# Optimization experiments

Measured on AMD Instinct MI355X. Metric: run time of the kernel, lower is better.

## Reference

```python
import jax, jax.numpy as jnp
import numpy as np

EMA_DECAY = 0.99
LAPLACE_EPS = 1e-7
PERPLEXITY_EPS = 1e-10
COMMIT_COEF = 0.25


def setup_inputs() -> dict:
    key = jax.random.key(0)
    k1, k2, k3, k4 = jax.random.split(key, 4)
    B, C, T, H, W = 8, 256, 4, 32, 32
    n_codes = 2048
    z = jax.random.normal(k1, (B, C, T, H, W), dtype=jnp.float32)
    embeddings = jax.random.normal(k2, (n_codes, C), dtype=jnp.float32)
    N = jnp.ones((n_codes,), dtype=jnp.float32)  # state after _init_embeddings
    z_avg = jax.random.normal(k3, (n_codes, C), dtype=jnp.float32)
    k_rand = jax.random.normal(k4, (n_codes, C), dtype=jnp.float32)  # stand-in for randperm restart rows
    return {"z": z, "embeddings": embeddings, "N": N, "z_avg": z_avg, "k_rand": k_rand}


def reference(z, embeddings, N, z_avg, k_rand):
    b, c, t, h, w = z.shape
    n_codes = embeddings.shape[0]
    # rearrange 'b c t h w -> (b t h w) c'
    flat = jnp.transpose(z, (0, 2, 3, 4, 1)).reshape(-1, c)  # [Ntok, c]
    d2 = ((flat * flat).sum(axis=1, keepdims=True)
          - 2.0 * (flat @ embeddings.T)
          + (embeddings * embeddings).sum(axis=1)[None, :])  # [Ntok, n_codes]
    idx = jnp.argmin(d2, axis=1)  # [Ntok] int
    quant_flat = embeddings[idx]  # gather, [Ntok, c]
    # back to [b, c, t, h, w] (the double-rearrange in the torch code is a net permute back)
    quant = jnp.transpose(quant_flat.reshape(b, t, h, w, c), (0, 4, 1, 2, 3))
    commitment_loss = COMMIT_COEF * jnp.mean((z - jax.lax.stop_gradient(quant)) ** 2)
    embeddings_st = jax.lax.stop_gradient(quant - z) + z  # straight-through
    # EMA codebook update (one-hot scatter expressed as segment_sum)
    ones = jnp.ones(flat.shape[0], dtype=flat.dtype)
    counts = jax.ops.segment_sum(ones, idx, num_segments=n_codes)          # n_total
    encode_sum = jax.ops.segment_sum(flat, idx, num_segments=n_codes)      # [n_codes, c]
    new_N = N * EMA_DECAY + (1.0 - EMA_DECAY) * counts
    new_z_avg = z_avg * EMA_DECAY + (1.0 - EMA_DECAY) * encode_sum
    n = new_N.sum()
    weights = (new_N + LAPLACE_EPS) / (n + n_codes * LAPLACE_EPS) * n
    new_embeddings = new_z_avg / weights[:, None]
    usage = (new_N[:, None] >= 1.0).astype(flat.dtype)
    new_embeddings = new_embeddings * usage + k_rand * (1.0 - usage)
    # perplexity
    avg_probs = counts / flat.shape[0]
    perplexity = jnp.exp(-jnp.sum(avg_probs * jnp.log(avg_probs + PERPLEXITY_EPS)))
    encodings = idx.reshape(b, t, h, w)
    return embeddings_st, encodings, commitment_loss, perplexity, new_embeddings, new_N, new_z_avg
```

## Files before the change

kernel.cpp:

```cpp
#include <hip/hip_runtime.h>
#include <math.h>

#define NCODES 2048
#define CDIM   256
#define SPAT   4096
#define NTOK   32768
#define XSTR   260
#define EPI_TOK 32

#define ETILE    32
#define HALFCODE 1024
#define NTILES   (HALFCODE / ETILE)

typedef _Float16 half8  __attribute__((ext_vector_type(8)));
typedef float    f32x4  __attribute__((ext_vector_type(4)));

#define WS_ENORM  0
#define WS_COUNTS 2048
#define WS_LOSS   4096
#define WS_N      4097
#define WS_ESUM   4100
#define WS_IDX    528388
#define WS_OFF    561156
#define WS_CUR    563204
#define WS_SORT   565252
#define WS_SCODE  598020
#define WS_CAND   630788
#define WS_E16    761860
#define WS_XH     1024004

#define O_QUANT 0
#define O_ENC   8388608
#define O_LOSS  8421376
#define O_PERP  8421377
#define O_EMB   8421378
#define O_NN    8945666
#define O_ZAVG  8947714

__device__ inline void gl_lds16(const void* g, void* l) {
    __builtin_amdgcn_global_load_lds(
        (const __attribute__((address_space(1))) void*)g,
        (__attribute__((address_space(3))) void*)l, 16, 0, 0);
}

__device__ inline unsigned umn(unsigned a, unsigned b) { return a < b ? a : b; }
__device__ inline unsigned umx(unsigned a, unsigned b) { return a > b ? a : b; }
__device__ inline unsigned shflx16(unsigned v, int off) {
    return (unsigned)__shfl_xor((int)v, off, 16);
}

__global__ void k_ecvt(const float* __restrict__ emb, float* __restrict__ ws) {
    const int tid  = threadIdx.x;
    const int code = (blockIdx.x << 3) + (tid >> 5);
    const int cg   = tid & 31;
    const float* src = emb + (size_t)code * CDIM + (cg << 3);
    const float4 f0 = *(const float4*)src;
    const float4 f1 = *(const float4*)(src + 4);
    half8 h = { (_Float16)f0.x, (_Float16)f0.y, (_Float16)f0.z, (_Float16)f0.w,
                (_Float16)f1.x, (_Float16)f1.y, (_Float16)f1.z, (_Float16)f1.w };
    char* dst = (char*)(ws + WS_E16) + (size_t)code * 512 + ((cg ^ (code & 7)) << 4);
    *(half8*)dst = h;
    float s = f0.x * f0.x + f0.y * f0.y + f0.z * f0.z + f0.w * f0.w
            + f1.x * f1.x + f1.y * f1.y + f1.z * f1.z + f1.w * f1.w;
#pragma unroll
    for (int off = 16; off; off >>= 1) s += __shfl_down(s, off, 32);
    if (cg == 0) ws[WS_ENORM + code] = s;
}

__global__ __launch_bounds__(256, 3) void k_main(
    const float* __restrict__ z, float* __restrict__ ws)
{
    __shared__ half8 Es8[2][ETILE][32];

    const int tid = threadIdx.x;
    const int blk = blockIdx.x;
    const int ch  = blk & 1;
    const int tb  = blk >> 1;
    const int b   = tb >> 5;
    const int s0  = (tb & 31) * 128;
    const float* zb = z + (size_t)b * CDIM * SPAT + s0;
    const char* e16g = (const char*)(ws + WS_E16) + (size_t)ch * HALFCODE * 512;

    const int l  = tid & 63, w = tid >> 6;
    const int lr = l & 15, lg = l >> 4;

    {
        char* dst = (char*)&Es8[0][0][0];
#pragma unroll
        for (int q = 0; q < 4; ++q) {
            const int off = ((q << 2) + w) << 10;
            gl_lds16(e16g + off + (l << 4), dst + off);
        }
    }

    half8 a[2][8];
#pragma unroll
    for (int as = 0; as < 2; ++as)
#pragma unroll
    for (int ks = 0; ks < 8; ++ks) {
        float v[8];
#pragma unroll
        for (int e = 0; e < 8; ++e)
            v[e] = zb[(size_t)(ks * 32 + lg * 8 + e) * SPAT + (w * 32 + as * 16 + lr)];
        half8 h = { (_Float16)v[0], (_Float16)v[1], (_Float16)v[2], (_Float16)v[3],
                    (_Float16)v[4], (_Float16)v[5], (_Float16)v[6], (_Float16)v[7] };
        a[as][ks] = h;
    }

    unsigned kb0[2][4], kb1[2][4];
#pragma unroll
    for (int as = 0; as < 2; ++as)
#pragma unroll
    for (int r = 0; r < 4; ++r) { kb0[as][r] = 0xFFFFFFFFu; kb1[as][r] = 0xFFFFFFFFu; }

    __syncthreads();

    int p = 0;
    for (int tile = 0; tile < NTILES; ++tile) {
        if (tile < NTILES - 1) {
            const char* src = e16g + (size_t)(tile + 1) * (ETILE * 512);
            char* dst = (char*)&Es8[p ^ 1][0][0];
#pragma unroll
            for (int q = 0; q < 4; ++q) {
                const int off = ((q << 2) + w) << 10;
                gl_lds16(src + off + (l << 4), dst + off);
            }
        }

        const float en0 = ws[WS_ENORM + ch * HALFCODE + tile * ETILE + lr];
        const float en1 = ws[WS_ENORM + ch * HALFCODE + tile * ETILE + 16 + lr];

        f32x4 acc[2][2];
#pragma unroll
        for (int as = 0; as < 2; ++as)
#pragma unroll
        for (int j = 0; j < 2; ++j) acc[as][j] = (f32x4)0.0f;

        half8 bf0[2], bf1[2];
#pragma unroll
        for (int j = 0; j < 2; ++j) {
            const int row = j * 16 + lr;
            bf0[j] = Es8[p][row][lg ^ (row & 7)];
        }
#pragma unroll
        for (int ks = 0; ks < 8; ++ks) {
            if (ks < 7) {
#pragma unroll
                for (int j = 0; j < 2; ++j) {
                    const int row = j * 16 + lr;
                    if (ks & 1) bf0[j] = Es8[p][row][((ks + 1) * 4 + lg) ^ (row & 7)];
                    else        bf1[j] = Es8[p][row][((ks + 1) * 4 + lg) ^ (row & 7)];
                }
            }
            __builtin_amdgcn_s_setprio(1);
#pragma unroll
            for (int as = 0; as < 2; ++as)
#pragma unroll
            for (int j = 0; j < 2; ++j)
                acc[as][j] = __builtin_amdgcn_mfma_f32_16x16x32_f16(
                    a[as][ks], (ks & 1) ? bf1[j] : bf0[j], acc[as][j], 0, 0, 0);
            __builtin_amdgcn_s_setprio(0);
        }

        const float enb0 = en0 + 4096.0f;
        const float enb1 = en1 + 4096.0f;
        const unsigned code0 = (unsigned)(ch * HALFCODE + tile * ETILE + lr);
        const unsigned code1 = code0 + 16u;
#pragma unroll
        for (int as = 0; as < 2; ++as)
#pragma unroll
        for (int r = 0; r < 4; ++r) {
            {
                const float d = fmaf(acc[as][0][r], -2.0f, enb0);
                const unsigned key = (__float_as_uint(d) & 0xFFFFF800u) | code0;
                const unsigned hi = umx(kb0[as][r], key);
                kb0[as][r] = umn(kb0[as][r], key);
                kb1[as][r] = umn(kb1[as][r], hi);
            }
            {
                const float d = fmaf(acc[as][1][r], -2.0f, enb1);
                const unsigned key = (__float_as_uint(d) & 0xFFFFF800u) | code1;
                const unsigned hi = umx(kb0[as][r], key);
                kb0[as][r] = umn(kb0[as][r], key);
                kb1[as][r] = umn(kb1[as][r], hi);
            }
        }

        __syncthreads();
        p ^= 1;
    }

#pragma unroll
    for (int as = 0; as < 2; ++as)
#pragma unroll
    for (int r = 0; r < 4; ++r) {
        unsigned k0 = kb0[as][r], k1 = kb1[as][r];
        unsigned k2 = 0xFFFFFFFFu, k3 = 0xFFFFFFFFu;
#pragma unroll
        for (int off = 8; off; off >>= 1) {
            const unsigned o0 = shflx16(k0, off);
            const unsigned o1 = shflx16(k1, off);
            const unsigned o2 = shflx16(k2, off);
            const unsigned o3 = shflx16(k3, off);
            const unsigned m0 = umn(k0, o3), m1 = umn(k1, o2);
            const unsigned m2 = umn(k2, o1), m3 = umn(k3, o0);
            const unsigned t0 = umn(m0, m2), t2 = umx(m0, m2);
            const unsigned t1 = umn(m1, m3), t3 = umx(m1, m3);
            k0 = umn(t0, t1); k1 = umx(t0, t1);
            k2 = umn(t2, t3); k3 = umx(t2, t3);
        }
        if (lr == 0) {
            const int tokg = b * SPAT + s0 + w * 32 + as * 16 + lg * 4 + r;
            ushort4 c4;
            c4.x = (unsigned short)(k0 & 2047u);
            c4.y = (unsigned short)(k1 & 2047u);
            c4.z = (unsigned short)(k2 & 2047u);
            c4.w = (unsigned short)(k3 & 2047u);
            *(ushort4*)((unsigned short*)((int*)ws + WS_CAND) + (size_t)tokg * 8 + ch * 4) = c4;
        }
    }
}

__global__ __launch_bounds__(256, 4) void k_epi(
    const float* __restrict__ z, const float* __restrict__ emb,
    float* __restrict__ ws, float* __restrict__ out)
{
    __shared__ float Xs[EPI_TOK * XSTR];
    __shared__ int   idxs[EPI_TOK];

    const int tid = threadIdx.x, blk = blockIdx.x;
    const int b   = blk >> 7;
    const int s0  = (blk & 127) * EPI_TOK;
    const float* zb = z + (size_t)b * CDIM * SPAT + s0;

    {
        const int s  = tid & 31;
        const int c0 = tid >> 5;
#pragma unroll 4
        for (int c = c0; c < CDIM; c += 8)
            Xs[s * XSTR + c] = zb[(size_t)c * SPAT + s];
    }
    __syncthreads();

    {
        const int r  = tid >> 5;
        const int cg = tid & 31;
        _Float16* xh = (_Float16*)(ws + WS_XH) + (size_t)blk * EPI_TOK * CDIM;
#pragma unroll
        for (int t8 = 0; t8 < 4; ++t8) {
            const int t = t8 * 8 + r;
            const float* xr = &Xs[t * XSTR + (cg << 3)];
            const float4 f0 = *(const float4*)xr;
            const float4 f1 = *(const float4*)(xr + 4);
            half8 h = { (_Float16)f0.x, (_Float16)f0.y, (_Float16)f0.z, (_Float16)f0.w,
                        (_Float16)f1.x, (_Float16)f1.y, (_Float16)f1.z, (_Float16)f1.w };
            *(half8*)(xh + (size_t)t * CDIM + (cg << 3)) = h;
        }
    }

    {
        const int t = tid >> 3, h = tid & 7;
        const unsigned short* cp =
            (const unsigned short*)((int*)ws + WS_CAND) + ((size_t)blk * EPI_TOK + t) * 8;
        const int mycand = cp[h];
        const float en_h = ws[WS_ENORM + mycand];

        int cand[8];
        {
            const ushort4 ca = *(const ushort4*)cp;
            const ushort4 cb = *(const ushort4*)(cp + 4);
            cand[0] = ca.x; cand[1] = ca.y; cand[2] = ca.z; cand[3] = ca.w;
            cand[4] = cb.x; cand[5] = cb.y; cand[6] = cb.z; cand[7] = cb.w;
        }

        float4 xq[8];
#pragma unroll
        for (int q = 0; q < 8; ++q)
            xq[q] = *(const float4*)&Xs[t * XSTR + q * 32 + h * 4];

        float p8[8];
#pragma unroll
        for (int k = 0; k < 8; ++k) {
            const float* er = emb + (size_t)cand[k] * CDIM + h * 4;
            float dp = 0.0f;
#pragma unroll
            for (int q = 0; q < 8; ++q) {
                const float4 e4 = *(const float4*)(er + q * 32);
                dp += xq[q].x * e4.x + xq[q].y * e4.y + xq[q].z * e4.z + xq[q].w * e4.w;
            }
            p8[k] = dp;
        }

        float np4[4];
#pragma unroll
        for (int k2 = 0; k2 < 4; ++k2) {
            const float own = (h & 1) ? p8[2 * k2 + 1] : p8[2 * k2];
            const float snd = (h & 1) ? p8[2 * k2]     : p8[2 * k2 + 1];
            np4[k2] = own + __shfl_xor(snd, 1, 8);
        }
        float nq2[2];
#pragma unroll
        for (int k3 = 0; k3 < 2; ++k3) {
            const float own = ((h >> 1) & 1) ? np4[2 * k3 + 1] : np4[2 * k3];
            const float snd = ((h >> 1) & 1) ? np4[2 * k3]     : np4[2 * k3 + 1];
            nq2[k3] = own + __shfl_xor(snd, 2, 8);
        }
        const float own = ((h >> 2) & 1) ? nq2[1] : nq2[0];
        const float snd = ((h >> 2) & 1) ? nq2[0] : nq2[1];
        const float dot = own + __shfl_xor(snd, 4, 8);

        float bd = en_h - 2.0f * dot;
        int   bi = mycand;
#pragma unroll
        for (int off = 1; off < 8; off <<= 1) {
            const float od = __shfl_xor(bd, off, 8);
            const int   oi = __shfl_xor(bi, off, 8);
            if (od < bd || (od == bd && oi < bi)) { bd = od; bi = oi; }
        }
        if (h == 0) idxs[t] = bi;
    }
    __syncthreads();

    float lsum = 0.0f;
    {
        const int s  = tid & 31;
        const int c0 = tid >> 5;
        const int code = idxs[s];
        const float* erow = emb + (size_t)code * CDIM;
        float* qcol = out + O_QUANT + (size_t)b * CDIM * SPAT + s0 + s;
#pragma unroll 4
        for (int c = c0; c < CDIM; c += 8) {
            const float e = erow[c];
            const float x = Xs[s * XSTR + c];
            const float df = x - e;
            lsum += df * df;
            qcol[(size_t)c * SPAT] = e;
        }
    }
#pragma unroll
    for (int off = 32; off; off >>= 1) lsum += __shfl_down(lsum, off);
    if ((tid & 63) == 0) atomicAdd(ws + WS_LOSS, lsum);

    if (tid < EPI_TOK) {
        const int code = idxs[tid];
        out[O_ENC + blk * EPI_TOK + tid] = (float)code;
        ((int*)ws)[WS_IDX + blk * EPI_TOK + tid] = code;
        atomicAdd(ws + WS_COUNTS + code, 1.0f);
    }
}

__global__ void k_finalize(const float* __restrict__ Nin, float* __restrict__ ws,
                           float* __restrict__ out) {
    __shared__ float r1[4], r2[4];
    __shared__ int   wsum[4];
    const int tid  = threadIdx.x;
    const int base = tid * 8;

    float cnt[8];
    {
        const float4 c0 = *(const float4*)(ws + WS_COUNTS + base);
        const float4 c1 = *(const float4*)(ws + WS_COUNTS + base + 4);
        cnt[0] = c0.x; cnt[1] = c0.y; cnt[2] = c0.z; cnt[3] = c0.w;
        cnt[4] = c1.x; cnt[5] = c1.y; cnt[6] = c1.z; cnt[7] = c1.w;
    }

    float nsum = 0.0f, H = 0.0f;
    int   tsum = 0;
#pragma unroll
    for (int j = 0; j < 8; ++j) {
        const float cf = cnt[j];
        const float nn = Nin[base + j] * 0.99f + 0.01f * cf;
        out[O_NN + base + j] = nn;
        nsum += nn;
        const float p = cf * (1.0f / 32768.0f);
        H += p * logf(p + 1e-10f);
        tsum += (int)cf;
    }

    int inc = tsum;
#pragma unroll
    for (int off = 1; off < 64; off <<= 1) {
        const int v = __shfl_up(inc, off, 64);
        if ((tid & 63) >= off) inc += v;
    }
    const int wv = tid >> 6, ln = tid & 63;
    if (ln == 63) wsum[wv] = inc;

#pragma unroll
    for (int off = 32; off; off >>= 1) {
        nsum += __shfl_down(nsum, off);
        H    += __shfl_down(H, off);
    }
    if (ln == 0) { r1[wv] = nsum; r2[wv] = H; }
    __syncthreads();

    int wbase = 0;
    for (int q = 0; q < wv; ++q) wbase += wsum[q];
    int run = wbase + inc - tsum;
    int* offp = (int*)ws + WS_OFF;
    int* curp = (int*)ws + WS_CUR;
#pragma unroll
    for (int j = 0; j < 8; ++j) {
        offp[base + j] = run;
        curp[base + j] = run;
        run += (int)cnt[j];
    }

    if (tid == 0) {
        const float nt = r1[0] + r1[1] + r1[2] + r1[3];
        const float Ht = r2[0] + r2[1] + r2[2] + r2[3];
        ws[WS_N] = nt;
        out[O_PERP] = expf(-Ht);
        out[O_LOSS] = 0.25f * ws[WS_LOSS] * (1.0f / 8388608.0f);
    }
}

__global__ void k_scatter(float* __restrict__ ws) {
    const int t    = blockIdx.x * 256 + threadIdx.x;
    const int code = ((const int*)ws)[WS_IDX + t];
    const int slot = atomicAdd((int*)ws + WS_CUR + code, 1);
    ((int*)ws)[WS_SORT  + slot] = t;
    ((int*)ws)[WS_SCODE + slot] = code;
}

__global__ __launch_bounds__(256) void k_gather(float* __restrict__ ws) {
    __shared__ int stok[64], scod[64];
    const int g = blockIdx.x, tid = threadIdx.x, c = tid;
    if (tid < 64) {
        stok[tid] = ((const int*)ws)[WS_SORT  + g * 64 + tid];
        scod[tid] = ((const int*)ws)[WS_SCODE + g * 64 + tid];
    }
    __syncthreads();

    const _Float16* xh = (const _Float16*)(ws + WS_XH);
    float* esum = ws + WS_ESUM;

    float acc = 0.0f;
    for (int k0 = 0; k0 < 64; k0 += 8) {
        float v[8];
#pragma unroll
        for (int j = 0; j < 8; ++j)
            v[j] = (float)xh[(size_t)stok[k0 + j] * CDIM + c];
#pragma unroll
        for (int j = 0; j < 8; ++j) {
            const int k = k0 + j;
            acc += v[j];
            if (k == 63 || scod[k] != scod[k + 1]) {
                atomicAdd(&esum[(size_t)scod[k] * CDIM + c], acc);
                acc = 0.0f;
            }
        }
    }
}

__global__ __launch_bounds__(256) void k_update(
    const float* __restrict__ zavg, const float* __restrict__ krand,
    const float* __restrict__ ws, float* __restrict__ out)
{
    const int i = blockIdx.x, c = threadIdx.x;
    const float nn  = out[O_NN + i];
    const float n   = ws[WS_N];
    const float wgt = (nn + 1e-7f) / (n + NCODES * 1e-7f) * n;
    const size_t o  = (size_t)i * CDIM + c;
    const float ez  = 0.99f * zavg[o] + 0.01f * ws[WS_ESUM + o];
    out[O_ZAVG + o] = ez;
    out[O_EMB + o]  = (nn >= 1.0f) ? (ez / wgt) : krand[o];
}

extern "C" void kernel_launch(void* const* d_in, const int* in_sizes, int n_in,
                              void* d_out, int out_size, void* d_ws, size_t ws_size,
                              hipStream_t stream) {
    const float* z     = (const float*)d_in[0];
    const float* emb   = (const float*)d_in[1];
    const float* Nin   = (const float*)d_in[2];
    const float* zavg  = (const float*)d_in[3];
    const float* krand = (const float*)d_in[4];
    float* out = (float*)d_out;
    float* ws  = (float*)d_ws;

    hipMemsetAsync(ws + WS_COUNTS, 0,
                   (size_t)(2048 + 4 + NCODES * CDIM) * sizeof(float), stream);

    k_ecvt    <<<NCODES / 8,  256, 0, stream>>>(emb, ws);
    k_main    <<<512,         256, 0, stream>>>(z, ws);
    k_epi     <<<1024,        256, 0, stream>>>(z, emb, ws, out);
    k_finalize<<<1,           256, 0, stream>>>(Nin, ws, out);
    k_scatter <<<NTOK / 256,  256, 0, stream>>>(ws);
    k_gather  <<<NTOK / 64,   256, 0, stream>>>(ws);
    k_update  <<<NCODES,      256, 0, stream>>>(zavg, krand, ws, out);
}
```

Before: 165.7 us.

## Move fp16 token staging into main kernel and restructure epilogue loss and writes

The fp16 copy of the tokens is now written from the main distance kernel, which already holds them in registers, so the epilogue no longer converts and stores it. The epilogue handles 16 tokens per block with 16 lanes per token across twice as many blocks, and its launch bound rises to 6 blocks per unit. The commitment loss is now computed algebraically as ||x||^2 plus the best distance instead of re-reading the embedding row per element. The chosen rows are staged through LDS so the quant writes are coalesced. The algebraic loss uses the fp32 expansion, which can differ slightly in rounding from the direct squared difference.

```diff
diff --git a/kernel.cpp b/kernel.cpp
--- a/kernel.cpp
+++ b/kernel.cpp
@@ -6,7 +6,7 @@
 #define SPAT   4096
 #define NTOK   32768
 #define XSTR   260
-#define EPI_TOK 32
+#define EPI_TOK 16
 
 #define ETILE    32
 #define HALFCODE 1024
@@ -105,6 +105,17 @@
         half8 h = { (_Float16)v[0], (_Float16)v[1], (_Float16)v[2], (_Float16)v[3],
                     (_Float16)v[4], (_Float16)v[5], (_Float16)v[6], (_Float16)v[7] };
         a[as][ks] = h;
+    }
+
+    if (ch == 0) {
+        _Float16* xh = (_Float16*)(ws + WS_XH);
+#pragma unroll
+        for (int as = 0; as < 2; ++as) {
+            _Float16* xr = xh + (size_t)(b * SPAT + s0 + w * 32 + as * 16 + lr) * CDIM;
+#pragma unroll
+            for (int ks = 0; ks < 8; ++ks)
+                *(half8*)(xr + ks * 32 + lg * 8) = a[as][ks];
+        }
     }
 
     unsigned kb0[2][4], kb1[2][4];
@@ -221,48 +232,33 @@
     }
 }
 
-__global__ __launch_bounds__(256, 4) void k_epi(
+__global__ __launch_bounds__(256, 6) void k_epi(
     const float* __restrict__ z, const float* __restrict__ emb,
     float* __restrict__ ws, float* __restrict__ out)
 {
     __shared__ float Xs[EPI_TOK * XSTR];
     __shared__ int   idxs[EPI_TOK];
+    __shared__ float lloss[EPI_TOK];
 
     const int tid = threadIdx.x, blk = blockIdx.x;
-    const int b   = blk >> 7;
-    const int s0  = (blk & 127) * EPI_TOK;
+    const int b   = blk >> 8;
+    const int s0  = (blk & 255) * EPI_TOK;
     const float* zb = z + (size_t)b * CDIM * SPAT + s0;
 
     {
-        const int s  = tid & 31;
-        const int c0 = tid >> 5;
+        const int s  = tid & 15;
+        const int c0 = tid >> 4;
 #pragma unroll 4
-        for (int c = c0; c < CDIM; c += 8)
+        for (int c = c0; c < CDIM; c += 16)
             Xs[s * XSTR + c] = zb[(size_t)c * SPAT + s];
     }
     __syncthreads();
 
     {
-        const int r  = tid >> 5;
-        const int cg = tid & 31;
-        _Float16* xh = (_Float16*)(ws + WS_XH) + (size_t)blk * EPI_TOK * CDIM;
-#pragma unroll
-        for (int t8 = 0; t8 < 4; ++t8) {
-            const int t = t8 * 8 + r;
-            const float* xr = &Xs[t * XSTR + (cg << 3)];
-            const float4 f0 = *(const float4*)xr;
-            const float4 f1 = *(const float4*)(xr + 4);
-            half8 h = { (_Float16)f0.x, (_Float16)f0.y, (_Float16)f0.z, (_Float16)f0.w,
-                        (_Float16)f1.x, (_Float16)f1.y, (_Float16)f1.z, (_Float16)f1.w };
-            *(half8*)(xh + (size_t)t * CDIM + (cg << 3)) = h;
-        }
-    }
-
-    {
-        const int t = tid >> 3, h = tid & 7;
+        const int t = tid >> 4, h = tid & 15, j = h & 7;
         const unsigned short* cp =
             (const unsigned short*)((int*)ws + WS_CAND) + ((size_t)blk * EPI_TOK + t) * 8;
-        const int mycand = cp[h];
+        const int mycand = cp[j];
         const float en_h = ws[WS_ENORM + mycand];
 
         int cand[8];
@@ -273,10 +269,16 @@
             cand[4] = cb.x; cand[5] = cb.y; cand[6] = cb.z; cand[7] = cb.w;
         }
 
-        float4 xq[8];
-#pragma unroll
-        for (int q = 0; q < 8; ++q)
-            xq[q] = *(const float4*)&Xs[t * XSTR + q * 32 + h * 4];
+        float4 xq[4];
+#pragma unroll
+        for (int q = 0; q < 4; ++q)
+            xq[q] = *(const float4*)&Xs[t * XSTR + q * 64 + h * 4];
+
+        float xn = 0.0f;
+#pragma unroll
+        for (int q = 0; q < 4; ++q)
+            xn += xq[q].x * xq[q].x + xq[q].y * xq[q].y
+                + xq[q].z * xq[q].z + xq[q].w * xq[q].w;
 
         float p8[8];
 #pragma unroll
@@ -284,68 +286,78 @@
             const float* er = emb + (size_t)cand[k] * CDIM + h * 4;
             float dp = 0.0f;
 #pragma unroll
-            for (int q = 0; q < 8; ++q) {
-                const float4 e4 = *(const float4*)(er + q * 32);
+            for (int q = 0; q < 4; ++q) {
+                const float4 e4 = *(const float4*)(er + q * 64);
                 dp += xq[q].x * e4.x + xq[q].y * e4.y + xq[q].z * e4.z + xq[q].w * e4.w;
             }
             p8[k] = dp;
         }
 
+#pragma unroll
+        for (int k = 0; k < 8; ++k) p8[k] += __shfl_xor(p8[k], 8, 16);
+        xn += __shfl_xor(xn, 8, 16);
+
         float np4[4];
 #pragma unroll
         for (int k2 = 0; k2 < 4; ++k2) {
             const float own = (h & 1) ? p8[2 * k2 + 1] : p8[2 * k2];
             const float snd = (h & 1) ? p8[2 * k2]     : p8[2 * k2 + 1];
-            np4[k2] = own + __shfl_xor(snd, 1, 8);
-        }
+            np4[k2] = own + __shfl_xor(snd, 1, 16);
+        }
+        xn += __shfl_xor(xn, 1, 16);
         float nq2[2];
 #pragma unroll
         for (int k3 = 0; k3 < 2; ++k3) {
             const float own = ((h >> 1) & 1) ? np4[2 * k3 + 1] : np4[2 * k3];
             const float snd = ((h >> 1) & 1) ? np4[2 * k3]     : np4[2 * k3 + 1];
-            nq2[k3] = own + __shfl_xor(snd, 2, 8);
-        }
+            nq2[k3] = own + __shfl_xor(snd, 2, 16);
+        }
+        xn += __shfl_xor(xn, 2, 16);
         const float own = ((h >> 2) & 1) ? nq2[1] : nq2[0];
         const float snd = ((h >> 2) & 1) ? nq2[0] : nq2[1];
-        const float dot = own + __shfl_xor(snd, 4, 8);
+        const float dot = own + __shfl_xor(snd, 4, 16);
+        xn += __shfl_xor(xn, 4, 16);
 
         float bd = en_h - 2.0f * dot;
         int   bi = mycand;
 #pragma unroll
-        for (int off = 1; off < 8; off <<= 1) {
-            const float od = __shfl_xor(bd, off, 8);
-            const int   oi = __shfl_xor(bi, off, 8);
+        for (int off = 1; off < 16; off <<= 1) {
+            const float od = __shfl_xor(bd, off, 16);
+            const int   oi = __shfl_xor(bi, off, 16);
             if (od < bd || (od == bd && oi < bi)) { bd = od; bi = oi; }
         }
-        if (h == 0) idxs[t] = bi;
+        if (h == 0) {
+            idxs[t]  = bi;
+            lloss[t] = xn + bd;
+            out[O_ENC + blk * EPI_TOK + t] = (float)bi;
+            ((int*)ws)[WS_IDX + blk * EPI_TOK + t] = bi;
+            atomicAdd(ws + WS_COUNTS + bi, 1.0f);
+        }
     }
     __syncthreads();
 
-    float lsum = 0.0f;
     {
-        const int s  = tid & 31;
-        const int c0 = tid >> 5;
-        const int code = idxs[s];
-        const float* erow = emb + (size_t)code * CDIM;
+        const int t = tid >> 4, h = tid & 15;
+        const float* ewin = emb + (size_t)idxs[t] * CDIM + h * 4;
+#pragma unroll
+        for (int q = 0; q < 4; ++q)
+            *(float4*)&Xs[t * XSTR + q * 64 + h * 4] = *(const float4*)(ewin + q * 64);
+    }
+    __syncthreads();
+
+    {
+        const int s  = tid & 15;
+        const int c0 = tid >> 4;
         float* qcol = out + O_QUANT + (size_t)b * CDIM * SPAT + s0 + s;
 #pragma unroll 4
-        for (int c = c0; c < CDIM; c += 8) {
-            const float e = erow[c];
-            const float x = Xs[s * XSTR + c];
-            const float df = x - e;
-            lsum += df * df;
-            qcol[(size_t)c * SPAT] = e;
-        }
-    }
-#pragma unroll
-    for (int off = 32; off; off >>= 1) lsum += __shfl_down(lsum, off);
-    if ((tid & 63) == 0) atomicAdd(ws + WS_LOSS, lsum);
-
-    if (tid < EPI_TOK) {
-        const int code = idxs[tid];
-        out[O_ENC + blk * EPI_TOK + tid] = (float)code;
-        ((int*)ws)[WS_IDX + blk * EPI_TOK + tid] = code;
-        atomicAdd(ws + WS_COUNTS + code, 1.0f);
+        for (int c = c0; c < CDIM; c += 16)
+            qcol[(size_t)c * SPAT] = Xs[s * XSTR + c];
+    }
+    if (tid == 0) {
+        float ls = 0.0f;
+#pragma unroll
+        for (int t = 0; t < EPI_TOK; ++t) ls += lloss[t];
+        atomicAdd(ws + WS_LOSS, ls);
     }
 }
 
@@ -483,7 +495,7 @@
 
     k_ecvt    <<<NCODES / 8,  256, 0, stream>>>(emb, ws);
     k_main    <<<512,         256, 0, stream>>>(z, ws);
-    k_epi     <<<1024,        256, 0, stream>>>(z, emb, ws, out);
+    k_epi     <<<2048,        256, 0, stream>>>(z, emb, ws, out);
     k_finalize<<<1,           256, 0, stream>>>(Nin, ws, out);
     k_scatter <<<NTOK / 256,  256, 0, stream>>>(ws);
     k_gather  <<<NTOK / 64,   256, 0, stream>>>(ws);
```

Measured after the change: 148.3 us. 1.12x faster.
